# Optimization experiments

Measured on AMD Instinct MI355X. Metric: run time of the kernel, lower is better.

The kernel has to match this reference:

```python
import math
import jax, jax.numpy as jnp
import numpy as np

B_SZ, N_TOK, D_MODEL, EXPAND, D_STATE = 4, 1024, 192, 2, 16
D_INNER = EXPAND * D_MODEL  # 384


def setup_inputs() -> dict:
    key = jax.random.key(0)
    ks = jax.random.split(key, 6)
    dt_init = math.log(math.exp(0.1) - 1.0)
    x = jax.random.normal(ks[0], (B_SZ, N_TOK, D_INNER), dtype=jnp.float32)
    # dt projection weights: uniform(-1e-4, 1e-4), bias = softplus-inverse(0.1)
    W_dts = jax.random.uniform(ks[1], (D_INNER, D_INNER), minval=-1e-4, maxval=1e-4, dtype=jnp.float32)
    W_dtd = jax.random.uniform(ks[2], (D_INNER, D_INNER), minval=-1e-4, maxval=1e-4, dtype=jnp.float32)
    b_dts = jnp.full((D_INNER,), dt_init, dtype=jnp.float32)
    b_dtd = jnp.full((D_INNER,), dt_init, dtype=jnp.float32)
    # B/C projections (no bias)
    W_B = jax.random.normal(ks[3], (D_STATE, D_INNER), dtype=jnp.float32) * 0.05
    W_C = jax.random.normal(ks[4], (D_STATE, D_INNER), dtype=jnp.float32) * 0.05
    D_param = jnp.ones((D_INNER,), dtype=jnp.float32)
    A_log = jnp.broadcast_to(jnp.log(jnp.arange(1, D_STATE + 1, dtype=jnp.float32))[None, :], (D_INNER, D_STATE))
    diff_raw = jnp.zeros((1, D_INNER, 1, 1), dtype=jnp.float32)
    return {"x": x, "W_dts": W_dts, "b_dts": b_dts, "W_dtd": W_dtd, "b_dtd": b_dtd,
            "W_B": W_B, "W_C": W_C, "D_param": D_param, "A_log": A_log,
            "diff_raw": diff_raw, "K_steps": 3}


def _laplacian(h, H, W):
    # h: (B, N, D, S); 5-point stencil with replicate (edge) padding, per (D,S) channel
    Bv, N, D, S = h.shape
    g = h.reshape(Bv, H, W, D, S)
    g = jnp.pad(g, ((0, 0), (1, 1), (1, 1), (0, 0), (0, 0)), mode='edge')
    lap = (g[:, 2:, 1:-1] + g[:, :-2, 1:-1] + g[:, 1:-1, 2:] + g[:, 1:-1, :-2]
           - 4.0 * g[:, 1:-1, 1:-1])
    return lap.reshape(Bv, N, D, S)


def reference(x, W_dts, b_dts, W_dtd, b_dtd, W_B, W_C, D_param, A_log, diff_raw, K_steps):
    Bv, N, D = x.shape
    H = Wd = int(math.sqrt(N))
    A = -jax.nn.softplus(A_log)                                   # (D, S), negative decay
    delta_s = jnp.minimum(jax.nn.softplus(x @ W_dts.T + b_dts), 0.15)  # (B, N, D)
    delta_d = jnp.minimum(jax.nn.softplus(x @ W_dtd.T + b_dtd), 0.15)  # (B, N, D)
    B_mat = x @ W_B.T                                             # (B, N, S)
    C_mat = x @ W_C.T                                             # (B, N, S)
    h0 = jnp.einsum('bnd,bns->bnds', x, B_mat)                    # (B, N, D, S)
    D_coeff = (jax.nn.sigmoid(diff_raw) * 0.5).reshape(1, 1, D, 1)
    dt = 1.0 / K_steps
    A_exp = A[None, None]            # (1, 1, D, S)
    ds_e = delta_s[..., None]        # (B, N, D, 1)
    dd_e = delta_d[..., None]
    h = h0
    for _ in range(K_steps):
        lap = _laplacian(h, H, Wd)
        h = h + dt * (ds_e * (A_exp * h + h0) + dd_e * D_coeff * lap)
    y = jnp.einsum('bnds,bns->bnd', h, C_mat) + x * D_param
    return y
```

## Files before the change

kernel.cpp:

```cpp
#include <hip/hip_runtime.h>
#include <hip/hip_bf16.h>

#define BSZ   4
#define NTOK  1024
#define DIN   384
#define DST   16
#define MROWS (BSZ * NTOK)
#define KDIM  384
#define NM    (MROWS * DIN)

typedef __attribute__((ext_vector_type(8))) short bf16x8;
typedef __attribute__((ext_vector_type(4))) float f32x4;

__device__ __forceinline__ float softplus_f(float z) {
  return (z > 20.0f) ? z : log1pf(expf(z));
}

__device__ __forceinline__ unsigned short f32_to_bf16(float f) {
  unsigned int u = __float_as_uint(f);
  unsigned int rnd = 0x7fffu + ((u >> 16) & 1u);
  return (unsigned short)((u + rnd) >> 16);
}

__device__ __forceinline__ float bf16_lo(unsigned int w) { return __uint_as_float(w << 16); }
__device__ __forceinline__ float bf16_hi(unsigned int w) { return __uint_as_float(w & 0xffff0000u); }

__global__ __launch_bounds__(256) void wconv_kernel(
    const float* __restrict__ Wdts, const float* __restrict__ Wdtd,
    const float* __restrict__ WB,   const float* __restrict__ WC,
    unsigned short* __restrict__ Wb)
{
  const int idx8 = (blockIdx.x * 256 + threadIdx.x) * 8;
  const int row = idx8 / KDIM;
  const int k   = idx8 % KDIM;
  uint4 o = make_uint4(0u, 0u, 0u, 0u);
  if (row < 800) {
    const float* src;
    if (row < 384)      src = Wdts + (long)row * KDIM + k;
    else if (row < 768) src = Wdtd + (long)(row - 384) * KDIM + k;
    else if (row < 784) src = WB   + (long)(row - 768) * KDIM + k;
    else                src = WC   + (long)(row - 784) * KDIM + k;
    float4 v0 = *(const float4*)src;
    float4 v1 = *(const float4*)(src + 4);
    o.x = (unsigned int)f32_to_bf16(v0.x) | ((unsigned int)f32_to_bf16(v0.y) << 16);
    o.y = (unsigned int)f32_to_bf16(v0.z) | ((unsigned int)f32_to_bf16(v0.w) << 16);
    o.z = (unsigned int)f32_to_bf16(v1.x) | ((unsigned int)f32_to_bf16(v1.y) << 16);
    o.w = (unsigned int)f32_to_bf16(v1.z) | ((unsigned int)f32_to_bf16(v1.w) << 16);
  }
  *(uint4*)&Wb[idx8] = o;
}

__global__ __launch_bounds__(256) void xpose_kernel(
    const float* __restrict__ x, float* __restrict__ xT,
    unsigned short* __restrict__ xb)
{
  __shared__ float tile[32][33];
  const int n0 = blockIdx.x * 32;
  const int d0 = blockIdx.y * 32;
  const int b  = blockIdx.z;
  const int tx = threadIdx.x & 31, ty = threadIdx.x >> 5;
#pragma unroll
  for (int i = 0; i < 4; ++i) {
    int nn = n0 + ty + i * 8;
    float v = x[(long)(b * NTOK + nn) * DIN + d0 + tx];
    tile[ty + i * 8][tx] = v;
    xb[(long)(b * NTOK + nn) * DIN + d0 + tx] = f32_to_bf16(v);
  }
  __syncthreads();
#pragma unroll
  for (int i = 0; i < 4; ++i) {
    int dd = d0 + ty + i * 8;
    xT[(long)(b * DIN + dd) * NTOK + n0 + tx] = tile[tx][ty + i * 8];
  }
}

__global__ __launch_bounds__(256) void proj_mfma_kernel(
    const unsigned short* __restrict__ xb,
    const unsigned short* __restrict__ Wb,
    const float* __restrict__ bdts, const float* __restrict__ bdtd,
    unsigned short* __restrict__ dsT, unsigned short* __restrict__ ddT,
    float* __restrict__ BT, float* __restrict__ CT)
{
  __shared__ short smem_s[2][2][64 * 72];

  const int t    = threadIdx.x;
  const int bm   = blockIdx.x & 63;
  const int bn   = blockIdx.x >> 6;
  const int row0 = bm * 64;
  const int col0 = bn * 64;
  const int bat  = row0 >> 10;
  const int n0   = row0 & 1023;

  const int l  = t & 63;
  const int w  = t >> 6;
  const int wr = (w >> 1) * 32;
  const int wc = (w & 1) * 32;
  const int lr = l & 15;
  const int lk = (l >> 4) * 8;

  const int sr = t >> 2;
  const int sk = (t & 3) * 16;

  f32x4 acc[2][2];
  const f32x4 zero = {0.f, 0.f, 0.f, 0.f};
  acc[0][0] = zero; acc[0][1] = zero; acc[1][0] = zero; acc[1][1] = zero;

  uint4 la0, la1, lw0, lw1;
#define PLOAD(K0)                                                          \
  {                                                                        \
    const unsigned short* ap = &xb[(long)(row0 + sr) * KDIM + (K0) + sk];  \
    const unsigned short* wp = &Wb[(long)(col0 + sr) * KDIM + (K0) + sk];  \
    la0 = *(const uint4*)ap;  la1 = *(const uint4*)(ap + 8);               \
    lw0 = *(const uint4*)wp;  lw1 = *(const uint4*)(wp + 8);               \
  }
#define PSTORE(BUF)                                                        \
  {                                                                        \
    *(uint4*)&smem_s[BUF][0][sr * 72 + sk]     = la0;                      \
    *(uint4*)&smem_s[BUF][0][sr * 72 + sk + 8] = la1;                      \
    *(uint4*)&smem_s[BUF][1][sr * 72 + sk]     = lw0;                      \
    *(uint4*)&smem_s[BUF][1][sr * 72 + sk + 8] = lw1;                      \
  }

  PLOAD(0);
  PSTORE(0);

  for (int it = 0; it < 6; ++it) {
    const int cur = it & 1;
    __syncthreads();
    if (it + 1 < 6) PLOAD((it + 1) * 64);
    const short* Asm = smem_s[cur][0];
    const short* Wsm = smem_s[cur][1];
#pragma unroll
    for (int kh = 0; kh < 2; ++kh) {
      const int ko = kh * 32 + lk;
      bf16x8 a0 = *(const bf16x8*)&Asm[(wr + lr) * 72 + ko];
      bf16x8 a1 = *(const bf16x8*)&Asm[(wr + 16 + lr) * 72 + ko];
      bf16x8 b0 = *(const bf16x8*)&Wsm[(wc + lr) * 72 + ko];
      bf16x8 b1 = *(const bf16x8*)&Wsm[(wc + 16 + lr) * 72 + ko];
      acc[0][0] = __builtin_amdgcn_mfma_f32_16x16x32_bf16(a0, b0, acc[0][0], 0, 0, 0);
      acc[0][1] = __builtin_amdgcn_mfma_f32_16x16x32_bf16(a0, b1, acc[0][1], 0, 0, 0);
      acc[1][0] = __builtin_amdgcn_mfma_f32_16x16x32_bf16(a1, b0, acc[1][0], 0, 0, 0);
      acc[1][1] = __builtin_amdgcn_mfma_f32_16x16x32_bf16(a1, b1, acc[1][1], 0, 0, 0);
    }
    if (it + 1 < 6) PSTORE(cur ^ 1);
  }

  if (bn < 12) {
    const float* bias = (bn < 6) ? bdts : bdtd;
    unsigned short* plane = (bn < 6) ? dsT : ddT;
    const int dbase = (bn < 6) ? col0 : col0 - 384;
    const float bv0 = bias[dbase + wc + lr];
    const float bv1 = bias[dbase + wc + 16 + lr];
    __syncthreads();
    unsigned short* outl = (unsigned short*)smem_s;
#pragma unroll
    for (int i = 0; i < 2; ++i)
#pragma unroll
      for (int j = 0; j < 2; ++j) {
        const float bb = j ? bv1 : bv0;
        const int cl = wc + j * 16 + lr;
#pragma unroll
        for (int q = 0; q < 4; ++q) {
          const int nl = wr + i * 16 + (l >> 4) * 4 + q;
          float dl = fminf(softplus_f(acc[i][j][q] + bb), 0.15f);
          outl[cl * 72 + nl] = f32_to_bf16(dl);
        }
      }
    __syncthreads();
    const int dl = t >> 2;
    const int seg = t & 3;
    uint4 w0 = *(const uint4*)&outl[dl * 72 + seg * 16];
    uint4 w1 = *(const uint4*)&outl[dl * 72 + seg * 16 + 8];
    long addr = (long)(bat * DIN + dbase + dl) * NTOK + n0 + seg * 16;
    *(uint4*)&plane[addr]     = w0;
    *(uint4*)&plane[addr + 8] = w1;
  } else {
#pragma unroll
    for (int i = 0; i < 2; ++i)
#pragma unroll
      for (int j = 0; j < 2; ++j) {
        const int cl = wc + j * 16 + lr;
        const int rowbase = row0 + wr + i * 16 + (l >> 4) * 4;
        if (cl < 16)       *(f32x4*)&BT[(long)cl * MROWS + rowbase] = acc[i][j];
        else if (cl < 32)  *(f32x4*)&CT[(long)(cl - 16) * MROWS + rowbase] = acc[i][j];
      }
  }
#undef PLOAD
#undef PSTORE
}

__global__ __launch_bounds__(1024) void ssm_kernel(
    const float* __restrict__ xT,
    const unsigned short* __restrict__ dsT,
    const unsigned short* __restrict__ ddT,
    const float* __restrict__ BT, const float* __restrict__ CT,
    const float* __restrict__ Dparam, const float* __restrict__ Alog,
    const float* __restrict__ diffraw, const int* __restrict__ Kp,
    float* __restrict__ yT)
{
  __shared__ float P[16 * 1024];
  const int t   = threadIdx.x;
  const int s   = t >> 6;
  const int l64 = t & 63;
  const int pr  = l64 >> 3, pc = l64 & 7;
  const int d = blockIdx.x % DIN;
  const int b = blockIdx.x / DIN;
  const int K = Kp[0];
  const float dt = 1.0f / (float)K;
  const float Dc = 0.5f / (1.0f + expf(-diffraw[d]));
  const float A  = -log1pf(expf(Alog[d * DST + s]));
  const float dtDc = dt * Dc;
  const long col = (long)(b * DIN + d) * NTOK;
  const long gr0 = (long)b * NTOK;
  const int  c0  = pc * 4;

  float h[16], cA[16], g0[16], a2v[16];
#pragma unroll
  for (int i = 0; i < 4; ++i) {
    const int n = (pr * 4 + i) * 32 + c0;
    float4 xv = *(const float4*)&xT[col + n];
    float4 bv = *(const float4*)&BT[(long)s * MROWS + gr0 + n];
    uint2 dsw = *(const uint2*)&dsT[col + n];
    uint2 ddw = *(const uint2*)&ddT[col + n];
    float dsf[4] = { bf16_lo(dsw.x), bf16_hi(dsw.x), bf16_lo(dsw.y), bf16_hi(dsw.y) };
    float ddf[4] = { bf16_lo(ddw.x), bf16_hi(ddw.x), bf16_lo(ddw.y), bf16_hi(ddw.y) };
    float xa[4] = { xv.x, xv.y, xv.z, xv.w };
    float ba[4] = { bv.x, bv.y, bv.z, bv.w };
#pragma unroll
    for (int j = 0; j < 4; ++j) {
      const int e = i * 4 + j;
      float a1 = dt * dsf[j];
      float a2 = dtDc * ddf[j];
      float h0 = xa[j] * ba[j];
      h[e]   = h0;
      g0[e]  = a1 * h0;
      a2v[e] = a2;
      cA[e]  = fmaf(a1, A, 1.0f) - 4.0f * a2;
    }
  }

  const int lu = (l64 - 8) & 63, ld = (l64 + 8) & 63;
  const int ll = (l64 - 1) & 63, lrr = (l64 + 1) & 63;

  for (int k = 0; k < K; ++k) {
    float up[4], dn[4], lf[4], rt[4];
#pragma unroll
    for (int j = 0; j < 4; ++j) {
      up[j] = __shfl(h[12 + j], lu);
      dn[j] = __shfl(h[j], ld);
      lf[j] = __shfl(h[4 * j + 3], ll);
      rt[j] = __shfl(h[4 * j], lrr);
    }
#pragma unroll
    for (int j = 0; j < 4; ++j) {
      up[j] = (pr == 0) ? h[j]          : up[j];
      dn[j] = (pr == 7) ? h[12 + j]     : dn[j];
      lf[j] = (pc == 0) ? h[4 * j]      : lf[j];
      rt[j] = (pc == 7) ? h[4 * j + 3]  : rt[j];
    }
    float hn[16];
#pragma unroll
    for (int i = 0; i < 4; ++i)
#pragma unroll
      for (int j = 0; j < 4; ++j) {
        const int e = i * 4 + j;
        float uv = (i == 0) ? up[j] : h[e - 4];
        float dv = (i == 3) ? dn[j] : h[e + 4];
        float lv = (j == 0) ? lf[i] : h[e - 1];
        float rv = (j == 3) ? rt[i] : h[e + 1];
        float S  = (uv + dv) + (lv + rv);
        hn[e] = fmaf(cA[e], h[e], fmaf(a2v[e], S, g0[e]));
      }
#pragma unroll
    for (int e = 0; e < 16; ++e) h[e] = hn[e];
  }

#pragma unroll
  for (int i = 0; i < 4; ++i) {
    const int n = (pr * 4 + i) * 32 + c0;
    float4 cv = *(const float4*)&CT[(long)s * MROWS + gr0 + n];
    float4 pv;
    pv.x = h[i * 4 + 0] * cv.x;
    pv.y = h[i * 4 + 1] * cv.y;
    pv.z = h[i * 4 + 2] * cv.z;
    pv.w = h[i * 4 + 3] * cv.w;
    *(float4*)&P[s * 1024 + n] = pv;
  }
  __syncthreads();

  {
    float sum = 0.f;
#pragma unroll
    for (int ss = 0; ss < 16; ++ss) sum += P[ss * 1024 + t];
    yT[col + t] = fmaf(xT[col + t], Dparam[d], sum);
  }
}

__global__ __launch_bounds__(256) void untranspose_kernel(
    const float* __restrict__ yT, float* __restrict__ out)
{
  __shared__ float tile[32][33];
  const int n0 = blockIdx.x * 32;
  const int d0 = blockIdx.y * 32;
  const int b  = blockIdx.z;
  const int tx = threadIdx.x & 31, ty = threadIdx.x >> 5;
#pragma unroll
  for (int i = 0; i < 4; ++i) {
    int dd = d0 + ty + i * 8;
    tile[ty + i * 8][tx] = yT[(long)(b * DIN + dd) * NTOK + n0 + tx];
  }
  __syncthreads();
#pragma unroll
  for (int i = 0; i < 4; ++i) {
    int nn = n0 + ty + i * 8;
    out[(long)(b * NTOK + nn) * DIN + d0 + tx] = tile[tx][ty + i * 8];
  }
}

extern "C" void kernel_launch(void* const* d_in, const int* in_sizes, int n_in,
                              void* d_out, int out_size, void* d_ws, size_t ws_size,
                              hipStream_t stream) {
  const float* x     = (const float*)d_in[0];
  const float* Wdts  = (const float*)d_in[1];
  const float* bdts  = (const float*)d_in[2];
  const float* Wdtd  = (const float*)d_in[3];
  const float* bdtd  = (const float*)d_in[4];
  const float* WB    = (const float*)d_in[5];
  const float* WC    = (const float*)d_in[6];
  const float* Dpar  = (const float*)d_in[7];
  const float* Alog  = (const float*)d_in[8];
  const float* diffr = (const float*)d_in[9];
  const int*   Kst   = (const int*)d_in[10];

  float* BT = (float*)d_ws;
  float* CT = BT + (long)DST * MROWS;
  float* xT = CT + (long)DST * MROWS;
  float* yT = xT + NM;
  unsigned short* xb = (unsigned short*)yT;
  unsigned short* Wb = xb + NM;

  unsigned short* dsT = (unsigned short*)d_out;
  unsigned short* ddT = dsT + NM;

  wconv_kernel<<<dim3(156), dim3(256), 0, stream>>>(Wdts, Wdtd, WB, WC, Wb);

  xpose_kernel<<<dim3(NTOK / 32, DIN / 32, BSZ), dim3(256), 0, stream>>>(x, xT, xb);

  proj_mfma_kernel<<<dim3(64 * 13), dim3(256), 0, stream>>>(
      xb, Wb, bdts, bdtd, dsT, ddT, BT, CT);

  ssm_kernel<<<dim3(BSZ * DIN), dim3(1024), 0, stream>>>(
      xT, dsT, ddT, BT, CT, Dpar, Alog, diffr, Kst, yT);

  untranspose_kernel<<<dim3(NTOK / 32, DIN / 32, BSZ), dim3(256), 0, stream>>>(
      yT, (float*)d_out);
}
```

Baseline: 74.69 us.

## Split SSM state dimension across two blocks with bf16 partial outputs

The SSM kernel now launches twice as many 512-thread blocks, each handling half of the 16 state channels. Each block writes a bf16 partial sum of its half. The untranspose kernel adds the two partials and folds in the x*D skip term. The aim is better occupancy and scheduling with smaller blocks and half the shared memory per block. The cost is two extra partial-output buffers, and bf16 rounding of the partial sums lowers output precision.

Measured after the change: 68.04 us. 8.9% less time.

```diff
diff --git a/kernel.cpp b/kernel.cpp
--- a/kernel.cpp
+++ b/kernel.cpp
@@ -189,22 +189,25 @@
 #undef PSTORE
 }
 
-__global__ __launch_bounds__(1024) void ssm_kernel(
+__global__ __launch_bounds__(512) void ssm_kernel(
     const float* __restrict__ xT,
     const unsigned short* __restrict__ dsT,
     const unsigned short* __restrict__ ddT,
     const float* __restrict__ BT, const float* __restrict__ CT,
-    const float* __restrict__ Dparam, const float* __restrict__ Alog,
+    const float* __restrict__ Alog,
     const float* __restrict__ diffraw, const int* __restrict__ Kp,
-    float* __restrict__ yT)
-{
-  __shared__ float P[16 * 1024];
+    unsigned short* __restrict__ yH0, unsigned short* __restrict__ yH1)
+{
+  __shared__ float P[8 * 1024];
+  const int bid   = blockIdx.x;
+  const int shalf = bid & 1;
+  const int bd    = bid >> 1;
+  const int d = bd % DIN;
+  const int b = bd / DIN;
   const int t   = threadIdx.x;
-  const int s   = t >> 6;
+  const int s   = shalf * 8 + (t >> 6);
   const int l64 = t & 63;
   const int pr  = l64 >> 3, pc = l64 & 7;
-  const int d = blockIdx.x % DIN;
-  const int b = blockIdx.x / DIN;
   const int K = Kp[0];
   const float dt = 1.0f / (float)K;
   const float Dc = 0.5f / (1.0f + expf(-diffraw[d]));
@@ -275,6 +278,7 @@
     for (int e = 0; e < 16; ++e) h[e] = hn[e];
   }
 
+  const int sw = t >> 6;
 #pragma unroll
   for (int i = 0; i < 4; ++i) {
     const int n = (pr * 4 + i) * 32 + c0;
@@ -284,20 +288,26 @@
     pv.y = h[i * 4 + 1] * cv.y;
     pv.z = h[i * 4 + 2] * cv.z;
     pv.w = h[i * 4 + 3] * cv.w;
-    *(float4*)&P[s * 1024 + n] = pv;
+    *(float4*)&P[sw * 1024 + n] = pv;
   }
   __syncthreads();
 
-  {
-    float sum = 0.f;
-#pragma unroll
-    for (int ss = 0; ss < 16; ++ss) sum += P[ss * 1024 + t];
-    yT[col + t] = fmaf(xT[col + t], Dparam[d], sum);
-  }
+  unsigned short* yH = shalf ? yH1 : yH0;
+  float s0 = 0.f, s1 = 0.f;
+#pragma unroll
+  for (int ss = 0; ss < 8; ++ss) {
+    s0 += P[ss * 1024 + t];
+    s1 += P[ss * 1024 + t + 512];
+  }
+  yH[col + t]       = f32_to_bf16(s0);
+  yH[col + t + 512] = f32_to_bf16(s1);
 }
 
 __global__ __launch_bounds__(256) void untranspose_kernel(
-    const float* __restrict__ yT, float* __restrict__ out)
+    const unsigned short* __restrict__ yH0,
+    const unsigned short* __restrict__ yH1,
+    const float* __restrict__ xT, const float* __restrict__ Dparam,
+    float* __restrict__ out)
 {
   __shared__ float tile[32][33];
   const int n0 = blockIdx.x * 32;
@@ -307,7 +317,10 @@
 #pragma unroll
   for (int i = 0; i < 4; ++i) {
     int dd = d0 + ty + i * 8;
-    tile[ty + i * 8][tx] = yT[(long)(b * DIN + dd) * NTOK + n0 + tx];
+    long idx = (long)(b * DIN + dd) * NTOK + n0 + tx;
+    float v0 = __uint_as_float((unsigned int)yH0[idx] << 16);
+    float v1 = __uint_as_float((unsigned int)yH1[idx] << 16);
+    tile[ty + i * 8][tx] = v0 + v1 + xT[idx] * Dparam[dd];
   }
   __syncthreads();
 #pragma unroll
@@ -335,9 +348,10 @@
   float* BT = (float*)d_ws;
   float* CT = BT + (long)DST * MROWS;
   float* xT = CT + (long)DST * MROWS;
-  float* yT = xT + NM;
-  unsigned short* xb = (unsigned short*)yT;
-  unsigned short* Wb = xb + NM;
+  unsigned short* yH0 = (unsigned short*)(xT + NM);
+  unsigned short* yH1 = yH0 + NM;
+  unsigned short* xb  = yH0;
+  unsigned short* Wb  = xb + NM;
 
   unsigned short* dsT = (unsigned short*)d_out;
   unsigned short* ddT = dsT + NM;
@@ -349,9 +363,9 @@
   proj_mfma_kernel<<<dim3(64 * 13), dim3(256), 0, stream>>>(
       xb, Wb, bdts, bdtd, dsT, ddT, BT, CT);
 
-  ssm_kernel<<<dim3(BSZ * DIN), dim3(1024), 0, stream>>>(
-      xT, dsT, ddT, BT, CT, Dpar, Alog, diffr, Kst, yT);
+  ssm_kernel<<<dim3(BSZ * DIN * 2), dim3(512), 0, stream>>>(
+      xT, dsT, ddT, BT, CT, Alog, diffr, Kst, yH0, yH1);
 
   untranspose_kernel<<<dim3(NTOK / 32, DIN / 32, BSZ), dim3(256), 0, stream>>>(
-      yT, (float*)d_out);
-}
+      yH0, yH1, xT, Dpar, (float*)d_out);
+}
```
